# Kernel tuning notes

Measured on AMD Instinct MI355X. Metric: run time of the kernel, lower is better.

The kernel has to match this reference:

```python
import jax, jax.numpy as jnp
import numpy as np

ALPHA = 0.2  # LeakyReLU negative slope

def setup_inputs() -> dict:
    key = jax.random.key(0)
    k1, k2, k3, k4 = jax.random.split(key, 4)
    B, N, IN_C, OUT_C = 4, 4096, 64, 64
    features = jax.random.normal(k1, (B, N, IN_C), dtype=jnp.float32)
    adj = jax.random.uniform(k2, (B, N, N), dtype=jnp.float32)  # unused by the module's math
    # xavier_normal approximations
    W = jax.random.normal(k3, (IN_C, OUT_C), dtype=jnp.float32) * np.sqrt(2.0 / (IN_C + OUT_C))
    a = jax.random.normal(k4, (2 * OUT_C, 1), dtype=jnp.float32) * np.sqrt(2.0 / (2 * OUT_C + 1))
    return {"features": features, "adj": adj, "W": W, "a": a}

def reference(features, adj, W, a):
    # h: [B, N, F]
    h = jnp.matmul(features, W)
    out_c = W.shape[1]
    a1 = a[:out_c, 0]   # [F]
    a2 = a[out_c:, 0]   # [F]
    # e[b,i,j] = leakyrelu(h_i . a1 + h_j . a2)  (decomposed; avoids O(N^2*2F) concat)
    s1 = jnp.einsum('bnf,f->bn', h, a1)  # [B, N]
    s2 = jnp.einsum('bnf,f->bn', h, a2)  # [B, N]
    e = s1[:, :, None] + s2[:, None, :]  # [B, N, N]
    e = jnp.where(e >= 0, e, ALPHA * e)  # leaky relu
    attention = jax.nn.softmax(e, axis=2)  # note: adj is NOT used (faithful to source)
    h_prime = jnp.matmul(attention, h)  # [B, N, F]
    return h_prime
```

## Files before the change

kernel.cpp:

```cpp
#include <hip/hip_runtime.h>
#include <hip/hip_bf16.h>
#include <cmath>

#define LRALPHA 0.2f

namespace {
constexpr int BB = 4;
constexpr int NN = 4096;
constexpr int ROWS = BB * NN;
}

typedef __attribute__((ext_vector_type(8))) short bf16x8;
typedef __attribute__((ext_vector_type(4))) float f32x4;

static __device__ inline short f2bf(float x) {
  __hip_bfloat16 t = __float2bfloat16(x);
  return *reinterpret_cast<short*>(&t);
}
static __device__ inline float bf2f(short x) {
  __hip_bfloat16 t = *reinterpret_cast<__hip_bfloat16*>(&x);
  return __bfloat162float(t);
}
static __device__ inline unsigned int packRNE(float a, float b) {
  unsigned int ua = __float_as_uint(a), ub = __float_as_uint(b);
  unsigned int ra = ua + 0x7FFFu + ((ua >> 16) & 1u);
  unsigned int rb = ub + 0x7FFFu + ((ub >> 16) & 1u);
  return (ra >> 16) | (rb & 0xFFFF0000u);
}

__global__ __launch_bounds__(256) void k_hcvt(
    const float* __restrict__ feat, const float* __restrict__ W,
    const float* __restrict__ a,
    unsigned short* __restrict__ hTh, unsigned short* __restrict__ hTl,
    float* __restrict__ Ag, float* __restrict__ Apg, float* __restrict__ Tg,
    float* __restrict__ Bv, float* __restrict__ Bpv) {
  __shared__ float tile[64][65];
  const int lane = threadIdx.x & 63;
  const int wave = threadIdx.x >> 6;
  const int row0 = blockIdx.x * 64;

  float wreg[64];
#pragma unroll
  for (int k = 0; k < 64; ++k) wreg[k] = W[k * 64 + lane];
  const float a1 = a[lane], a2 = a[64 + lane];

  for (int r = 0; r < 16; ++r) {
    const int row = row0 + wave * 16 + r;
    const float4* f4 = (const float4*)(feat + (size_t)row * 64);
    float hv = 0.f;
#pragma unroll
    for (int kk = 0; kk < 16; ++kk) {
      float4 f = f4[kk];
      hv = fmaf(f.x, wreg[4 * kk + 0], hv);
      hv = fmaf(f.y, wreg[4 * kk + 1], hv);
      hv = fmaf(f.z, wreg[4 * kk + 2], hv);
      hv = fmaf(f.w, wreg[4 * kk + 3], hv);
    }
    tile[wave * 16 + r][lane] = hv;
    float p1 = hv * a1, p2 = hv * a2;
#pragma unroll
    for (int off = 32; off; off >>= 1) {
      p1 += __shfl_xor(p1, off, 64);
      p2 += __shfl_xor(p2, off, 64);
    }
    if (lane == 0) {
      Ag[row]  = expf(p1);
      Apg[row] = expf(LRALPHA * p1);
      Tg[row]  = expf(-p1);
      Bv[row]  = expf(p2);
      Bpv[row] = expf(LRALPHA * p2);
    }
  }
  __syncthreads();

  const int b = row0 >> 12;
  const int n0 = row0 & (NN - 1);
#pragma unroll
  for (int cc = 0; cc < 16; ++cc) {
    int ch = cc * 4 + wave;
    float v = tile[lane][ch];
    short hi = f2bf(v);
    short lo = f2bf(v - bf2f(hi));
    size_t idx = ((size_t)(b * 64 + ch) << 12) + n0 + lane;
    hTh[idx] = (unsigned short)hi;
    hTl[idx] = (unsigned short)lo;
  }
}

__global__ __launch_bounds__(512, 4) void k_attn(
    const unsigned short* __restrict__ hTh, const unsigned short* __restrict__ hTl,
    const float* __restrict__ Ag, const float* __restrict__ Apg,
    const float* __restrict__ Tg,
    const float* __restrict__ Bv, const float* __restrict__ Bpv,
    float* __restrict__ out) {
  __shared__ float slab[4][32][65];
  __shared__ float l_lds[4][32];

  const int wave = threadIdx.x >> 6;
  const int lane = threadIdx.x & 63;
  const int m = lane & 15;
  const int quad = lane >> 4;
  const int row0 = blockIdx.x * 32;
  const int b = row0 >> 12;
  const int i0 = row0 + m, i1 = row0 + 16 + m;

  const float Ar0 = Ag[i0], Ap0 = Apg[i0], T0 = Tg[i0];
  const float Ar1 = Ag[i1], Ap1 = Apg[i1], T1 = Tg[i1];

  f32x4 acc00 = {0,0,0,0}, acc01 = {0,0,0,0}, acc02 = {0,0,0,0}, acc03 = {0,0,0,0};
  f32x4 acc10 = {0,0,0,0}, acc11 = {0,0,0,0}, acc12 = {0,0,0,0}, acc13 = {0,0,0,0};
  f32x4 lacc0 = {0,0,0,0}, lacc1 = {0,0,0,0};

  bf16x8 ones;
#pragma unroll
  for (int e = 0; e < 8; ++e) ones[e] = (short)0x3F80;

  const int j0 = wave * (NN / 8) + quad * 8;
  const float4* Bq4  = (const float4*)(Bv  + (b << 12) + j0);
  const float4* Bpq4 = (const float4*)(Bpv + (b << 12) + j0);
  const unsigned short* hp = hTh + ((size_t)(b * 64 + m) << 12) + j0;
  const unsigned short* lp = hTl + ((size_t)(b * 64 + m) << 12) + j0;
  constexpr size_t CH16 = (size_t)16 << 12;
  constexpr int ITERS = NN / 8 / 32;

  float4 bA = Bq4[0], bB = Bq4[1];
  float4 pA = Bpq4[0], pB = Bpq4[1];

  for (int it = 0; it < ITERS; ++it) {
    Bq4 += 8; Bpq4 += 8;
    float4 nbA = Bq4[0], nbB = Bq4[1];
    float4 npA = Bpq4[0], npB = Bpq4[1];

    bf16x8 hh0 = *(const bf16x8*)(hp);
    bf16x8 hh1 = *(const bf16x8*)(hp + CH16);
    bf16x8 hh2 = *(const bf16x8*)(hp + 2 * CH16);
    bf16x8 hh3 = *(const bf16x8*)(hp + 3 * CH16);
    bf16x8 hl0 = *(const bf16x8*)(lp);
    bf16x8 hl1 = *(const bf16x8*)(lp + CH16);
    bf16x8 hl2 = *(const bf16x8*)(lp + 2 * CH16);
    bf16x8 hl3 = *(const bf16x8*)(lp + 3 * CH16);

    float bvv[8] = {bA.x, bA.y, bA.z, bA.w, bB.x, bB.y, bB.z, bB.w};
    float pvv[8] = {pA.x, pA.y, pA.z, pA.w, pB.x, pB.y, pB.z, pB.w};

    float w0v[8], w1v[8];
#pragma unroll
    for (int e = 0; e < 8; ++e) {
      float Bj = bvv[e], Bpj = pvv[e];
      w0v[e] = (Bj >= T0) ? (Ar0 * Bj) : (Ap0 * Bpj);
      w1v[e] = (Bj >= T1) ? (Ar1 * Bj) : (Ap1 * Bpj);
    }
    union { bf16x8 v; unsigned int u[4]; } af0u, af1u;
#pragma unroll
    for (int p = 0; p < 4; ++p) {
      af0u.u[p] = packRNE(w0v[2 * p], w0v[2 * p + 1]);
      af1u.u[p] = packRNE(w1v[2 * p], w1v[2 * p + 1]);
    }
    bf16x8 af0 = af0u.v, af1 = af1u.v;

    lacc0 = __builtin_amdgcn_mfma_f32_16x16x32_bf16(af0, ones, lacc0, 0, 0, 0);
    lacc1 = __builtin_amdgcn_mfma_f32_16x16x32_bf16(af1, ones, lacc1, 0, 0, 0);
    acc00 = __builtin_amdgcn_mfma_f32_16x16x32_bf16(af0, hh0, acc00, 0, 0, 0);
    acc00 = __builtin_amdgcn_mfma_f32_16x16x32_bf16(af0, hl0, acc00, 0, 0, 0);
    acc01 = __builtin_amdgcn_mfma_f32_16x16x32_bf16(af0, hh1, acc01, 0, 0, 0);
    acc01 = __builtin_amdgcn_mfma_f32_16x16x32_bf16(af0, hl1, acc01, 0, 0, 0);
    acc02 = __builtin_amdgcn_mfma_f32_16x16x32_bf16(af0, hh2, acc02, 0, 0, 0);
    acc02 = __builtin_amdgcn_mfma_f32_16x16x32_bf16(af0, hl2, acc02, 0, 0, 0);
    acc03 = __builtin_amdgcn_mfma_f32_16x16x32_bf16(af0, hh3, acc03, 0, 0, 0);
    acc03 = __builtin_amdgcn_mfma_f32_16x16x32_bf16(af0, hl3, acc03, 0, 0, 0);
    acc10 = __builtin_amdgcn_mfma_f32_16x16x32_bf16(af1, hh0, acc10, 0, 0, 0);
    acc10 = __builtin_amdgcn_mfma_f32_16x16x32_bf16(af1, hl0, acc10, 0, 0, 0);
    acc11 = __builtin_amdgcn_mfma_f32_16x16x32_bf16(af1, hh1, acc11, 0, 0, 0);
    acc11 = __builtin_amdgcn_mfma_f32_16x16x32_bf16(af1, hl1, acc11, 0, 0, 0);
    acc12 = __builtin_amdgcn_mfma_f32_16x16x32_bf16(af1, hh2, acc12, 0, 0, 0);
    acc12 = __builtin_amdgcn_mfma_f32_16x16x32_bf16(af1, hl2, acc12, 0, 0, 0);
    acc13 = __builtin_amdgcn_mfma_f32_16x16x32_bf16(af1, hh3, acc13, 0, 0, 0);
    acc13 = __builtin_amdgcn_mfma_f32_16x16x32_bf16(af1, hl3, acc13, 0, 0, 0);

    hp += 32; lp += 32;
    bA = nbA; bB = nbB; pA = npA; pB = npB;
  }

  const int sidx = wave & 3;
  if (wave < 4) {
#pragma unroll
    for (int reg = 0; reg < 4; ++reg) {
      int rl = quad * 4 + reg;
      slab[sidx][rl][m]      = acc00[reg];
      slab[sidx][rl][m + 16] = acc01[reg];
      slab[sidx][rl][m + 32] = acc02[reg];
      slab[sidx][rl][m + 48] = acc03[reg];
      slab[sidx][16 + rl][m]      = acc10[reg];
      slab[sidx][16 + rl][m + 16] = acc11[reg];
      slab[sidx][16 + rl][m + 32] = acc12[reg];
      slab[sidx][16 + rl][m + 48] = acc13[reg];
    }
    if (m == 0) {
#pragma unroll
      for (int reg = 0; reg < 4; ++reg) {
        l_lds[sidx][quad * 4 + reg]      = lacc0[reg];
        l_lds[sidx][16 + quad * 4 + reg] = lacc1[reg];
      }
    }
  }
  __syncthreads();
  if (wave >= 4) {
#pragma unroll
    for (int reg = 0; reg < 4; ++reg) {
      int rl = quad * 4 + reg;
      slab[sidx][rl][m]      += acc00[reg];
      slab[sidx][rl][m + 16] += acc01[reg];
      slab[sidx][rl][m + 32] += acc02[reg];
      slab[sidx][rl][m + 48] += acc03[reg];
      slab[sidx][16 + rl][m]      += acc10[reg];
      slab[sidx][16 + rl][m + 16] += acc11[reg];
      slab[sidx][16 + rl][m + 32] += acc12[reg];
      slab[sidx][16 + rl][m + 48] += acc13[reg];
    }
    if (m == 0) {
#pragma unroll
      for (int reg = 0; reg < 4; ++reg) {
        l_lds[sidx][quad * 4 + reg]      += lacc0[reg];
        l_lds[sidx][16 + quad * 4 + reg] += lacc1[reg];
      }
    }
  }
  __syncthreads();

#pragma unroll
  for (int k = 0; k < 4; ++k) {
    int f = threadIdx.x + 512 * k;
    int rl = f >> 6, c = f & 63;
    float s = slab[0][rl][c] + slab[1][rl][c] + slab[2][rl][c] + slab[3][rl][c];
    float L = l_lds[0][rl] + l_lds[1][rl] + l_lds[2][rl] + l_lds[3][rl];
    out[((size_t)(row0 + rl)) * 64 + c] = s / L;
  }
}


extern "C" void kernel_launch(void* const* d_in, const int* in_sizes, int n_in,
                              void* d_out, int out_size, void* d_ws, size_t ws_size,
                              hipStream_t stream) {
  const float* feat = (const float*)d_in[0];
  const float* W = (const float*)d_in[2];
  const float* a = (const float*)d_in[3];
  float* out = (float*)d_out;

  char* ws = (char*)d_ws;
  size_t off = 0;
  auto carve = [&](size_t bytes) -> char* {
    char* p = ws + off;
    off = (off + bytes + 255) & ~(size_t)255;
    return p;
  };
  unsigned short* hTh = (unsigned short*)carve((size_t)ROWS * 64 * sizeof(unsigned short));
  unsigned short* hTl = (unsigned short*)carve((size_t)ROWS * 64 * sizeof(unsigned short));
  float* Ag    = (float*)carve(ROWS * sizeof(float));
  float* Apg   = (float*)carve(ROWS * sizeof(float));
  float* Tg    = (float*)carve(ROWS * sizeof(float));
  float* Bv    = (float*)carve((ROWS + 64) * sizeof(float));
  float* Bpv   = (float*)carve((ROWS + 64) * sizeof(float));

  k_hcvt<<<ROWS / 64, 256, 0, stream>>>(feat, W, a, hTh, hTl, Ag, Apg, Tg, Bv, Bpv);
  k_attn<<<ROWS / 32, 512, 0, stream>>>(hTh, hTl, Ag, Apg, Tg, Bv, Bpv, out);
}
```

Before: 391.1 us.

## Block hT into 8-element channel-interleaved tiles and use fmax for LeakyReLU weights

The transposed h buffers (high/low bf16 halves) are re-laid out so that each group of 8 consecutive j positions for all 64 channels forms one contiguous 1 KB block. The attention kernel's per-lane 16-byte loads for four channel groups then fall within that block instead of being 128 KB apart. The LeakyReLU branch, which compared against a precomputed exp(-s1) threshold, is replaced by fmaxf of the two exponential products. This is valid because exp is monotonic and leaky-relu equals max(x, 0.2x), and it removes the Tg array and its loads. The new layout shortens the strides of the main-loop memory access, at the cost of a less regular store pattern in the conversion kernel.

```diff
diff --git a/kernel.cpp b/kernel.cpp
--- a/kernel.cpp
+++ b/kernel.cpp
@@ -32,7 +32,7 @@
     const float* __restrict__ feat, const float* __restrict__ W,
     const float* __restrict__ a,
     unsigned short* __restrict__ hTh, unsigned short* __restrict__ hTl,
-    float* __restrict__ Ag, float* __restrict__ Apg, float* __restrict__ Tg,
+    float* __restrict__ Ag, float* __restrict__ Apg,
     float* __restrict__ Bv, float* __restrict__ Bpv) {
   __shared__ float tile[64][65];
   const int lane = threadIdx.x & 63;
@@ -66,7 +66,6 @@
     if (lane == 0) {
       Ag[row]  = expf(p1);
       Apg[row] = expf(LRALPHA * p1);
-      Tg[row]  = expf(-p1);
       Bv[row]  = expf(p2);
       Bpv[row] = expf(LRALPHA * p2);
     }
@@ -75,13 +74,15 @@
 
   const int b = row0 >> 12;
   const int n0 = row0 & (NN - 1);
+  const size_t base = ((size_t)b << 18) + ((size_t)(n0 >> 3) << 9)
+                    + ((size_t)(lane >> 3) << 9) + (lane & 7);
 #pragma unroll
   for (int cc = 0; cc < 16; ++cc) {
     int ch = cc * 4 + wave;
     float v = tile[lane][ch];
     short hi = f2bf(v);
     short lo = f2bf(v - bf2f(hi));
-    size_t idx = ((size_t)(b * 64 + ch) << 12) + n0 + lane;
+    size_t idx = base + (ch << 3);
     hTh[idx] = (unsigned short)hi;
     hTl[idx] = (unsigned short)lo;
   }
@@ -90,7 +91,6 @@
 __global__ __launch_bounds__(512, 4) void k_attn(
     const unsigned short* __restrict__ hTh, const unsigned short* __restrict__ hTl,
     const float* __restrict__ Ag, const float* __restrict__ Apg,
-    const float* __restrict__ Tg,
     const float* __restrict__ Bv, const float* __restrict__ Bpv,
     float* __restrict__ out) {
   __shared__ float slab[4][32][65];
@@ -104,8 +104,8 @@
   const int b = row0 >> 12;
   const int i0 = row0 + m, i1 = row0 + 16 + m;
 
-  const float Ar0 = Ag[i0], Ap0 = Apg[i0], T0 = Tg[i0];
-  const float Ar1 = Ag[i1], Ap1 = Apg[i1], T1 = Tg[i1];
+  const float Ar0 = Ag[i0], Ap0 = Apg[i0];
+  const float Ar1 = Ag[i1], Ap1 = Apg[i1];
 
   f32x4 acc00 = {0,0,0,0}, acc01 = {0,0,0,0}, acc02 = {0,0,0,0}, acc03 = {0,0,0,0};
   f32x4 acc10 = {0,0,0,0}, acc11 = {0,0,0,0}, acc12 = {0,0,0,0}, acc13 = {0,0,0,0};
@@ -118,9 +118,10 @@
   const int j0 = wave * (NN / 8) + quad * 8;
   const float4* Bq4  = (const float4*)(Bv  + (b << 12) + j0);
   const float4* Bpq4 = (const float4*)(Bpv + (b << 12) + j0);
-  const unsigned short* hp = hTh + ((size_t)(b * 64 + m) << 12) + j0;
-  const unsigned short* lp = hTl + ((size_t)(b * 64 + m) << 12) + j0;
-  constexpr size_t CH16 = (size_t)16 << 12;
+  const unsigned short* hp = hTh + ((size_t)b << 18)
+                           + ((size_t)(j0 >> 3) << 9) + (m << 3);
+  const unsigned short* lp = hTl + ((size_t)b << 18)
+                           + ((size_t)(j0 >> 3) << 9) + (m << 3);
   constexpr int ITERS = NN / 8 / 32;
 
   float4 bA = Bq4[0], bB = Bq4[1];
@@ -132,13 +133,13 @@
     float4 npA = Bpq4[0], npB = Bpq4[1];
 
     bf16x8 hh0 = *(const bf16x8*)(hp);
-    bf16x8 hh1 = *(const bf16x8*)(hp + CH16);
-    bf16x8 hh2 = *(const bf16x8*)(hp + 2 * CH16);
-    bf16x8 hh3 = *(const bf16x8*)(hp + 3 * CH16);
+    bf16x8 hh1 = *(const bf16x8*)(hp + 128);
+    bf16x8 hh2 = *(const bf16x8*)(hp + 256);
+    bf16x8 hh3 = *(const bf16x8*)(hp + 384);
     bf16x8 hl0 = *(const bf16x8*)(lp);
-    bf16x8 hl1 = *(const bf16x8*)(lp + CH16);
-    bf16x8 hl2 = *(const bf16x8*)(lp + 2 * CH16);
-    bf16x8 hl3 = *(const bf16x8*)(lp + 3 * CH16);
+    bf16x8 hl1 = *(const bf16x8*)(lp + 128);
+    bf16x8 hl2 = *(const bf16x8*)(lp + 256);
+    bf16x8 hl3 = *(const bf16x8*)(lp + 384);
 
     float bvv[8] = {bA.x, bA.y, bA.z, bA.w, bB.x, bB.y, bB.z, bB.w};
     float pvv[8] = {pA.x, pA.y, pA.z, pA.w, pB.x, pB.y, pB.z, pB.w};
@@ -147,8 +148,8 @@
 #pragma unroll
     for (int e = 0; e < 8; ++e) {
       float Bj = bvv[e], Bpj = pvv[e];
-      w0v[e] = (Bj >= T0) ? (Ar0 * Bj) : (Ap0 * Bpj);
-      w1v[e] = (Bj >= T1) ? (Ar1 * Bj) : (Ap1 * Bpj);
+      w0v[e] = fmaxf(Ar0 * Bj, Ap0 * Bpj);
+      w1v[e] = fmaxf(Ar1 * Bj, Ap1 * Bpj);
     }
     union { bf16x8 v; unsigned int u[4]; } af0u, af1u;
 #pragma unroll
@@ -177,7 +178,7 @@
     acc13 = __builtin_amdgcn_mfma_f32_16x16x32_bf16(af1, hh3, acc13, 0, 0, 0);
     acc13 = __builtin_amdgcn_mfma_f32_16x16x32_bf16(af1, hl3, acc13, 0, 0, 0);
 
-    hp += 32; lp += 32;
+    hp += 2048; lp += 2048;
     bA = nbA; bB = nbB; pA = npA; pB = npB;
   }
 
@@ -257,10 +258,9 @@
   unsigned short* hTl = (unsigned short*)carve((size_t)ROWS * 64 * sizeof(unsigned short));
   float* Ag    = (float*)carve(ROWS * sizeof(float));
   float* Apg   = (float*)carve(ROWS * sizeof(float));
-  float* Tg    = (float*)carve(ROWS * sizeof(float));
   float* Bv    = (float*)carve((ROWS + 64) * sizeof(float));
   float* Bpv   = (float*)carve((ROWS + 64) * sizeof(float));
 
-  k_hcvt<<<ROWS / 64, 256, 0, stream>>>(feat, W, a, hTh, hTl, Ag, Apg, Tg, Bv, Bpv);
-  k_attn<<<ROWS / 32, 512, 0, stream>>>(hTh, hTl, Ag, Apg, Tg, Bv, Bpv, out);
-}
+  k_hcvt<<<ROWS / 64, 256, 0, stream>>>(feat, W, a, hTh, hTl, Ag, Apg, Bv, Bpv);
+  k_attn<<<ROWS / 32, 512, 0, stream>>>(hTh, hTl, Ag, Apg, Bv, Bpv, out);
+}
```

Result: faster. 353.9 us (-9.5%).
